# Optimization experiments

Hardware: AMD Instinct MI355X
Metric: run time of the kernel (lower is better)

Reference implementation:

```python
import jax, jax.numpy as jnp
import numpy as np

B, S, D = 2, 2048, 2048
H, KV, HD = 32, 8, 64
REP = H // KV
THETA = 10000.0


def _rope_tables(seq_len, head_dim, dtype):
    inv_freq = 1.0 / (THETA ** (jnp.arange(0, head_dim, 2, dtype=jnp.float32) / head_dim))
    t = jnp.arange(seq_len, dtype=jnp.float32)
    freqs = jnp.outer(t, inv_freq)  # [S, HD/2]
    return jnp.cos(freqs).astype(dtype), jnp.sin(freqs).astype(dtype)


def _apply_rope(x, cos, sin):
    # x: [B, S, nh, HD]; cos/sin: [S, HD/2] -> broadcast [1, S, 1, HD/2]
    c = cos[None, :, None, :]
    s = sin[None, :, None, :]
    x1, x2 = x[..., : HD // 2], x[..., HD // 2:]
    return jnp.concatenate([x1 * c - x2 * s, x1 * s + x2 * c], axis=-1)


def setup_inputs() -> dict:
    key = jax.random.key(0)
    ks = jax.random.split(key, 5)
    x = jax.random.normal(ks[0], (B, S, D), dtype=jnp.float32)
    wq = jax.random.normal(ks[1], (D, H * HD), dtype=jnp.float32) * 0.02
    wk = jax.random.normal(ks[2], (D, KV * HD), dtype=jnp.float32) * 0.02
    wv = jax.random.normal(ks[3], (D, KV * HD), dtype=jnp.float32) * 0.02
    wo = jax.random.normal(ks[4], (H * HD, D), dtype=jnp.float32) * 0.02
    return {"x": x, "wq": wq, "wk": wk, "wv": wv, "wo": wo}


def reference(x, wq, wk, wv, wo):
    b, s, _ = x.shape
    q = (x @ wq).reshape(b, s, H, HD)
    k = (x @ wk).reshape(b, s, KV, HD)
    v = (x @ wv).reshape(b, s, KV, HD)

    cos, sin = _rope_tables(s, HD, x.dtype)
    q = _apply_rope(q, cos, sin)
    k = _apply_rope(k, cos, sin)

    # GQA: group query heads by KV head instead of repeating K/V (same math).
    qg = q.reshape(b, s, KV, REP, HD)  # [B,S,G,R,HD]
    scale = HD ** -0.5
    # scores: [B, G, R, Sq, Sk]
    scores = jnp.einsum("bsgrd,btgd->bgrst", qg, k) * scale
    causal = jnp.tril(jnp.ones((s, s), dtype=bool))
    scores = jnp.where(causal[None, None, None], scores, jnp.finfo(scores.dtype).min)
    probs = jax.nn.softmax(scores, axis=-1)
    out = jnp.einsum("bgrst,btgd->bsgrd", probs, v)  # [B,S,G,R,HD]
    out = out.reshape(b, s, H * HD)
    return out @ wo
```

## Files before the change

kernel.cpp:

```cpp
#include <hip/hip_runtime.h>

#define S_LEN 2048
#define NH 32
#define NKV 8
#define HEADD 64
#define DMODEL 2048
#define NQKV 3072

typedef float f32x4 __attribute__((ext_vector_type(4)));
typedef float f32x16 __attribute__((ext_vector_type(16)));
typedef short s16x8 __attribute__((ext_vector_type(8)));
typedef int   i32x4 __attribute__((ext_vector_type(4)));
typedef unsigned short u16;
typedef u16 u16x4 __attribute__((ext_vector_type(4)));

__device__ __forceinline__ float b2f(u16 u) {
  unsigned int x = ((unsigned int)u) << 16;
  float f;
  __builtin_memcpy(&f, &x, 4);
  return f;
}
__device__ __forceinline__ u16 f2b(float f) {
  unsigned int x;
  __builtin_memcpy(&x, &f, 4);
  unsigned int r = x + 0x7fffu + ((x >> 16) & 1u);
  return (u16)(r >> 16);
}
__device__ __forceinline__ unsigned fbits(float f) {
  unsigned x; __builtin_memcpy(&x, &f, 4); return x;
}

__device__ __forceinline__ void gload_lds16(const u16* g, u16* l) {
  __builtin_amdgcn_global_load_lds((const __attribute__((address_space(1))) void*)g,
                                   (__attribute__((address_space(3))) void*)l, 16, 0, 0);
}

template<int N> __device__ __forceinline__ void wait_vm() {
  asm volatile("s_waitcnt vmcnt(%0)" :: "n"(N) : "memory");
}

__global__ void cast_x_kernel(const float* __restrict__ src, u16* __restrict__ dst) {
  int i = (blockIdx.x * 256 + threadIdx.x) * 4;
  f32x4 v = *(const f32x4*)(src + i);
  u16x4 o;
  o[0] = f2b(v[0]); o[1] = f2b(v[1]); o[2] = f2b(v[2]); o[3] = f2b(v[3]);
  *(u16x4*)(dst + i) = o;
}

__global__ void transpose_cast(const float* __restrict__ src, u16* __restrict__ dst, int N, int K) {
  __shared__ float tile[32][33];
  int n0 = blockIdx.x * 32, k0 = blockIdx.y * 32;
  int tx = threadIdx.x, ty = threadIdx.y;
#pragma unroll
  for (int i = 0; i < 32; i += 8)
    tile[ty + i][tx] = src[(size_t)(k0 + ty + i) * N + n0 + tx];
  __syncthreads();
#pragma unroll
  for (int i = 0; i < 32; i += 8)
    dst[(size_t)(n0 + ty + i) * K + k0 + tx] = f2b(tile[tx][ty + i]);
}

#define PIPE_BODY(Q, STAGE, VMN)                                                   \
  {                                                                                \
    wait_vm<VMN>();                                                                \
    __builtin_amdgcn_s_barrier();                                                  \
    __builtin_amdgcn_sched_barrier(0);                                             \
    if (STAGE) {                                                                   \
      u16* db = sm + ((Q + 3) & 3) * BUFE;                                         \
      gload_lds16(gA0, db + w * 1024);                                             \
      gload_lds16(gA1, db + w * 1024 + 512);                                       \
      if (BN == 256) {                                                             \
        gload_lds16(gB0, db + ABUF + w * 1024);                                    \
        gload_lds16(gB1, db + ABUF + w * 1024 + 512);                              \
      } else {                                                                     \
        gload_lds16(gB0, db + ABUF + w * 512);                                     \
      }                                                                            \
      gA0 += 32; gA1 += 32; gB0 += 32; if (BN == 256) gB1 += 32;                   \
    }                                                                              \
    const u16* bb = sm + Q * BUFE;                                                 \
    s16x8 af[8], bf[NF];                                                           \
    _Pragma("unroll") for (int i = 0; i < 8; i++)  af[i] = *(const s16x8*)(bb + aoff[i]); \
    _Pragma("unroll") for (int j = 0; j < NF; j++) bf[j] = *(const s16x8*)(bb + boff[j]); \
    __builtin_amdgcn_s_setprio(1);                                                 \
    _Pragma("unroll") for (int mi = 0; mi < 8; mi++)                               \
      _Pragma("unroll") for (int ni = 0; ni < NF; ni++)                            \
        acc[mi][ni] = __builtin_amdgcn_mfma_f32_16x16x32_bf16(af[mi], bf[ni], acc[mi][ni], 0, 0, 0); \
    __builtin_amdgcn_s_setprio(0);                                                 \
  }

template<int BN>
__global__ __launch_bounds__(512, 2) void gemm_pipe(
    const u16* __restrict__ A, const u16* __restrict__ Bt, void* __restrict__ Cout,
    int M, int N, int writeF32) {
  extern __shared__ __align__(16) u16 sm[];
  constexpr int NF   = BN / 64;
  constexpr int ABUF = 256 * 32;
  constexpr int BUFE = ABUF + BN * 32;
  constexpr int LPS  = 2 + BN / 128;

  int nb = N / BN;
  int nwg = (M >> 8) * nb;
  int cpx = nwg >> 3;
  int bid = ((int)blockIdx.x & 7) * cpx + ((int)blockIdx.x >> 3);
  int m0 = (bid / nb) << 8;
  int n0 = (bid % nb) * BN;

  int tid = threadIdx.x;
  int lane = tid & 63;
  int w = tid >> 6;
  int wm8 = (w >> 2) << 7;
  int wn8 = (w & 3) * (BN / 4);
  int l15 = lane & 15;
  int quad = lane >> 4;

  int lr = lane >> 3;
  int lc = lane & 7;
  int slot = lc ^ lr;
  int kc8 = (slot & 3) << 3;
  const u16* gA0 = A + (size_t)(m0 + w * 32 + (lr << 1) + (slot >> 2)) * 2048 + kc8;
  const u16* gA1 = gA0 + (size_t)16 * 2048;
  const u16* gB0;
  const u16* gB1;
  if (BN == 256) {
    gB0 = Bt + (size_t)(n0 + w * 32 + (lr << 1) + (slot >> 2)) * 2048 + kc8;
    gB1 = gB0 + (size_t)16 * 2048;
  } else {
    gB0 = Bt + (size_t)(n0 + w * 16 + (lr << 1) + (slot >> 2)) * 2048 + kc8;
    gB1 = gB0;
  }

  int rb = l15 >> 1;
  int sl = (((((l15 & 1) << 2) | quad) ^ rb)) << 3;
  int rbase = rb * 64 + sl;
  int aoff[8], boff[NF];
#pragma unroll
  for (int i = 0; i < 8; i++) aoff[i] = wm8 * 32 + i * 512 + rbase;
#pragma unroll
  for (int j = 0; j < NF; j++) boff[j] = ABUF + wn8 * 32 + j * 512 + rbase;

  f32x4 acc[8][NF] = {};

#pragma unroll
  for (int pt = 0; pt < 3; pt++) {
    u16* db = sm + pt * BUFE;
    gload_lds16(gA0, db + w * 1024);
    gload_lds16(gA1, db + w * 1024 + 512);
    if (BN == 256) {
      gload_lds16(gB0, db + ABUF + w * 1024);
      gload_lds16(gB1, db + ABUF + w * 1024 + 512);
    } else {
      gload_lds16(gB0, db + ABUF + w * 512);
    }
    gA0 += 32; gA1 += 32; gB0 += 32; if (BN == 256) gB1 += 32;
  }

#pragma unroll 1
  for (int it = 0; it < 15; ++it) {
    PIPE_BODY(0, 1, 2 * LPS)
    PIPE_BODY(1, 1, 2 * LPS)
    PIPE_BODY(2, 1, 2 * LPS)
    PIPE_BODY(3, 1, 2 * LPS)
  }
  PIPE_BODY(0, 1, 2 * LPS)
  PIPE_BODY(1, 0, 2 * LPS)
  PIPE_BODY(2, 0, LPS)
  PIPE_BODY(3, 0, 0)

#pragma unroll
  for (int mi = 0; mi < 8; mi++)
#pragma unroll
    for (int ni = 0; ni < NF; ni++)
#pragma unroll
      for (int r = 0; r < 4; r++) {
        int row = m0 + wm8 + mi * 16 + (quad << 2) + r;
        int col = n0 + wn8 + ni * 16 + l15;
        float v = acc[mi][ni][r];
        if (writeF32) ((float*)Cout)[(size_t)row * N + col] = v;
        else ((u16*)Cout)[(size_t)row * N + col] = f2b(v);
      }
}

__global__ void rope_kernel(u16* __restrict__ qkv) {
  int row = blockIdx.x;
  int s = row & (S_LEN - 1);
  u16* p = qkv + (size_t)row * NQKV;
  int t = threadIdx.x;
  int d = t & 31;
  int hh = t >> 5;
  float inv_freq = exp2f(-(float)d * (13.287712379549449f / 32.0f));
  float ang = (float)s * inv_freq;
  float sn, cs;
  sincosf(ang, &sn, &cs);
  const float QSCALE = 0.18033688011112042f;
#pragma unroll
  for (int i = 0; i < 4; i++) {
    int base = (hh + (i << 3)) * HEADD + d;
    float x1 = b2f(p[base]);
    float x2 = b2f(p[base + 32]);
    p[base]      = f2b((x1 * cs - x2 * sn) * QSCALE);
    p[base + 32] = f2b((x1 * sn + x2 * cs) * QSCALE);
  }
  {
    int base = DMODEL + hh * HEADD + d;
    float x1 = b2f(p[base]);
    float x2 = b2f(p[base + 32]);
    p[base]      = f2b(x1 * cs - x2 * sn);
    p[base + 32] = f2b(x1 * sn + x2 * cs);
  }
}

__global__ void vtrans_kernel(const u16* __restrict__ qkv, u16* __restrict__ Vt) {
  __shared__ __align__(16) u16 tile[64][72];
  int bid = blockIdx.x;
  int st = bid & 31;
  int g  = (bid >> 5) & 7;
  int b  = bid >> 8;
  int tid = threadIdx.x;
  int r = tid >> 2;
  int c = (tid & 3) << 4;
  const u16* src = qkv + (size_t)(b * S_LEN + st * 64 + r) * NQKV + 2560 + g * 64 + c;
  *(i32x4*)&tile[r][c]     = *(const i32x4*)src;
  *(i32x4*)&tile[r][c + 8] = *(const i32x4*)(src + 8);
  __syncthreads();
  u16* dst = Vt + (size_t)((b * 8 + g) * 64 + r) * S_LEN + st * 64 + c;
  u16 tmp[16];
#pragma unroll
  for (int j = 0; j < 16; j++) tmp[j] = tile[c + j][r];
  *(i32x4*)dst       = *(i32x4*)&tmp[0];
  *(i32x4*)(dst + 8) = *(i32x4*)&tmp[8];
}

__global__ __launch_bounds__(64) void kvpack_kernel(const u16* __restrict__ qkv,
                                                    const u16* __restrict__ Vt,
                                                    u16* __restrict__ Kp,
                                                    u16* __restrict__ Vp) {
  int bid = blockIdx.x;
  int kb = bid & 63;
  int bg = bid >> 6;
  int g = bg & 7;
  int b = bg >> 3;
  int lane = threadIdx.x;
  int l31 = lane & 31;
  int h2 = lane >> 5;

  const u16* kq = qkv + (size_t)(b * S_LEN + kb * 32 + l31) * NQKV + DMODEL + g * 64 + h2 * 8;
  u16* kdst = Kp + ((size_t)bid * 4) * 512 + lane * 8;
#pragma unroll
  for (int t = 0; t < 4; t++)
    *(i32x4*)(kdst + t * 512) = *(const i32x4*)(kq + t * 16);

  const u16* vq = Vt + (size_t)(bg * 64 + l31) * S_LEN + kb * 32 + h2 * 8;
  u16* vdst = Vp + ((size_t)bid * 4) * 512 + lane * 8;
  *(i32x4*)(vdst)        = *(const i32x4*)vq;
  *(i32x4*)(vdst + 512)  = *(const i32x4*)(vq + 16);
  *(i32x4*)(vdst + 1024) = *(const i32x4*)(vq + (size_t)32 * S_LEN);
  *(i32x4*)(vdst + 1536) = *(const i32x4*)(vq + (size_t)32 * S_LEN + 16);
}

__global__ __launch_bounds__(64) void attn_kernel(const u16* __restrict__ qkv,
                                                  const u16* __restrict__ Kp,
                                                  const u16* __restrict__ Vp,
                                                  u16* __restrict__ out) {
  int bid = blockIdx.x;
  int bh = bid & 63;
  int pr = bid >> 6;
  int h = bh & 31;
  int b = bh >> 5;
  int g = h >> 2;
  int bg = b * 8 + g;
  int lane = threadIdx.x;
  int l31 = lane & 31;
  int h2 = lane >> 5;

  const u16* kp = Kp + ((size_t)bg * 64) * 2048 + lane * 8;
  const u16* vp = Vp + ((size_t)bg * 64) * 2048 + lane * 8;

#pragma unroll 1
  for (int pass = 0; pass < 2; ++pass) {
    int qb = pass ? pr : (63 - pr);
    int q0 = qb << 5;

    const u16* qp = qkv + (size_t)(b * S_LEN + q0 + l31) * NQKV + h * HEADD + h2 * 8;
    s16x8 qf[4];
#pragma unroll
    for (int t = 0; t < 4; t++) qf[t] = *(const s16x8*)(qp + t * 16);

    float l_i = 0.f;
    f32x16 acc[2] = {};

    s16x8 kfa[4], vfa[4], kfb[4], vfb[4];

    auto loadkv = [&](int kb, s16x8 (&kf)[4], s16x8 (&vf)[4]) {
      const u16* kpp = kp + (size_t)kb * 2048;
      const u16* vpp = vp + (size_t)kb * 2048;
#pragma unroll
      for (int t = 0; t < 4; t++) {
        kf[t] = *(const s16x8*)(kpp + t * 512);
        vf[t] = *(const s16x8*)(vpp + t * 512);
      }
    };

    auto compute = [&](int kb, s16x8 (&kf)[4], s16x8 (&vf)[4]) {
      f32x16 sc = {};
      __builtin_amdgcn_s_setprio(1);
#pragma unroll
      for (int t = 0; t < 4; t++)
        sc = __builtin_amdgcn_mfma_f32_32x32x16_bf16(kf[t], qf[t], sc, 0, 0, 0);
      __builtin_amdgcn_s_setprio(0);

      float sv[16];
#pragma unroll
      for (int j = 0; j < 16; j++) sv[j] = sc[j];

      if (kb == qb) {
        int qg = q0 + l31;
#pragma unroll
        for (int j = 0; j < 16; j++) {
          int kg = kb * 32 + (j & 3) + ((j >> 2) << 3) + (h2 << 2);
          if (kg > qg) sv[j] = -1e30f;
        }
      }

      float e[16];
#pragma unroll
      for (int j = 0; j < 16; j++) e[j] = __builtin_amdgcn_exp2f(sv[j]);

      float ps = (((e[0] + e[1]) + (e[2] + e[3])) + ((e[4] + e[5]) + (e[6] + e[7])))
               + (((e[8] + e[9]) + (e[10] + e[11])) + ((e[12] + e[13]) + (e[14] + e[15])));
      ps += __shfl_xor(ps, 32);
      l_i += ps;

      unsigned Pk[8], Ex[8];
#pragma unroll
      for (int r = 0; r < 8; r++) {
        unsigned pk;
        asm("v_cvt_pk_bf16_f32 %0, %1, %2" : "=v"(pk) : "v"(e[2 * r]), "v"(e[2 * r + 1]));
        Pk[r] = pk;
      }
#pragma unroll
      for (int r = 0; r < 8; r++) Ex[r] = (unsigned)__shfl_xor((int)Pk[r], 32);

      unsigned B0u[4], B1u[4];
      B0u[0] = h2 ? Ex[2] : Pk[0];
      B0u[1] = h2 ? Ex[3] : Pk[1];
      B0u[2] = h2 ? Pk[2] : Ex[0];
      B0u[3] = h2 ? Pk[3] : Ex[1];
      B1u[0] = h2 ? Ex[6] : Pk[4];
      B1u[1] = h2 ? Ex[7] : Pk[5];
      B1u[2] = h2 ? Pk[6] : Ex[4];
      B1u[3] = h2 ? Pk[7] : Ex[5];
      s16x8 B0, B1;
      __builtin_memcpy(&B0, B0u, 16);
      __builtin_memcpy(&B1, B1u, 16);

      __builtin_amdgcn_s_setprio(1);
      acc[0] = __builtin_amdgcn_mfma_f32_32x32x16_bf16(vf[0], B0, acc[0], 0, 0, 0);
      acc[0] = __builtin_amdgcn_mfma_f32_32x32x16_bf16(vf[1], B1, acc[0], 0, 0, 0);
      acc[1] = __builtin_amdgcn_mfma_f32_32x32x16_bf16(vf[2], B0, acc[1], 0, 0, 0);
      acc[1] = __builtin_amdgcn_mfma_f32_32x32x16_bf16(vf[3], B1, acc[1], 0, 0, 0);
      __builtin_amdgcn_s_setprio(0);
    };

    loadkv(0, kfa, vfa);
    int kb = 0;
    while (true) {
      if (kb < qb) loadkv(kb + 1, kfb, vfb);
      compute(kb, kfa, vfa);
      if (++kb > qb) break;
      if (kb < qb) loadkv(kb + 1, kfa, vfa);
      compute(kb, kfb, vfb);
      if (++kb > qb) break;
    }

    float linv = 1.0f / l_i;
    u16* op = out + (size_t)(b * S_LEN + q0 + l31) * DMODEL + h * HEADD;
#pragma unroll
    for (int dt = 0; dt < 2; dt++)
#pragma unroll
      for (int rg = 0; rg < 4; rg++) {
        u16x4 t4;
#pragma unroll
        for (int j = 0; j < 4; j++) t4[j] = f2b(acc[dt][rg * 4 + j] * linv);
        *(u16x4*)(op + dt * 32 + rg * 8 + h2 * 4) = t4;
      }
  }
}

extern "C" void kernel_launch(void* const* d_in, const int* in_sizes, int n_in,
                              void* d_out, int out_size, void* d_ws, size_t ws_size,
                              hipStream_t stream) {
  const float* x  = (const float*)d_in[0];
  const float* wq = (const float*)d_in[1];
  const float* wk = (const float*)d_in[2];
  const float* wv = (const float*)d_in[3];
  const float* wo = (const float*)d_in[4];

  char* ws = (char*)d_ws;
  u16* xb    = (u16*)ws;
  u16* wqkvT = (u16*)(ws + 16777216);
  u16* woT   = (u16*)(ws + 16777216 + 12582912);
  u16* qkv   = (u16*)(ws + 16777216 + 12582912 + 8388608);
  u16* attnb = xb;
  u16* Vt    = wqkvT;
  u16* Kp    = (u16*)(ws + 16777216 + 4194304);
  u16* Vp    = (u16*)(ws + 16777216 + 8388608);

  hipFuncSetAttribute(reinterpret_cast<const void*>(gemm_pipe<256>),
                      hipFuncAttributeMaxDynamicSharedMemorySize, 131072);
  hipFuncSetAttribute(reinterpret_cast<const void*>(gemm_pipe<128>),
                      hipFuncAttributeMaxDynamicSharedMemorySize, 98304);

  cast_x_kernel<<<8192, 256, 0, stream>>>(x, xb);
  dim3 tb(32, 8);
  transpose_cast<<<dim3(64, 64), tb, 0, stream>>>(wq, wqkvT, 2048, 2048);
  transpose_cast<<<dim3(16, 64), tb, 0, stream>>>(wk, wqkvT + (size_t)2048 * 2048, 512, 2048);
  transpose_cast<<<dim3(16, 64), tb, 0, stream>>>(wv, wqkvT + (size_t)2560 * 2048, 512, 2048);
  transpose_cast<<<dim3(64, 64), tb, 0, stream>>>(wo, woT, 2048, 2048);

  gemm_pipe<256><<<192, 512, 131072, stream>>>(xb, wqkvT, qkv, 4096, NQKV, 0);
  rope_kernel<<<4096, 256, 0, stream>>>(qkv);
  vtrans_kernel<<<512, 256, 0, stream>>>(qkv, Vt);
  kvpack_kernel<<<1024, 64, 0, stream>>>(qkv, Vt, Kp, Vp);
  attn_kernel<<<2048, 64, 0, stream>>>(qkv, Kp, Vp, attnb);
  gemm_pipe<128><<<256, 512, 98304, stream>>>(attnb, woT, d_out, 4096, 2048, 1);
}
```

Measured before the change: 311.1 us.

## Split attention key range across two waves with LDS reduction

Each attention block now has two wavefronts that take the lower and upper halves of the causal key-block range for the same query tile, roughly halving the serial loop length per wave. After the loop, the second wave writes its partial accumulators and row sums to shared memory and the first wave adds them, normalises and stores the output. The reduction is a plain sum with no rescaling, which appears to rely on the softmax using no running-max correction. The change adds two barriers, about 8 KB of LDS per block and doubled register demand per block, in exchange for more parallelism on the long causal rows.

```diff
diff --git a/kernel.cpp b/kernel.cpp
--- a/kernel.cpp
+++ b/kernel.cpp
@@ -257,10 +257,12 @@
   *(i32x4*)(vdst + 1536) = *(const i32x4*)(vq + (size_t)32 * S_LEN + 16);
 }
 
-__global__ __launch_bounds__(64) void attn_kernel(const u16* __restrict__ qkv,
-                                                  const u16* __restrict__ Kp,
-                                                  const u16* __restrict__ Vp,
-                                                  u16* __restrict__ out) {
+__global__ __launch_bounds__(128, 4) void attn_kernel(const u16* __restrict__ qkv,
+                                                      const u16* __restrict__ Kp,
+                                                      const u16* __restrict__ Vp,
+                                                      u16* __restrict__ out) {
+  __shared__ float red[33 * 64];
+
   int bid = blockIdx.x;
   int bh = bid & 63;
   int pr = bid >> 6;
@@ -268,7 +270,9 @@
   int b = bh >> 5;
   int g = h >> 2;
   int bg = b * 8 + g;
-  int lane = threadIdx.x;
+  int tid = threadIdx.x;
+  int wv = tid >> 6;
+  int lane = tid & 63;
   int l31 = lane & 31;
   int h2 = lane >> 5;
 
@@ -279,6 +283,10 @@
   for (int pass = 0; pass < 2; ++pass) {
     int qb = pass ? pr : (63 - pr);
     int q0 = qb << 5;
+    int nt = qb + 1;
+    int h1 = (nt + 1) >> 1;
+    int k_lo = wv ? h1 : 0;
+    int k_hi = wv ? nt : h1;
 
     const u16* qp = qkv + (size_t)(b * S_LEN + q0 + l31) * NQKV + h * HEADD + h2 * 8;
     s16x8 qf[4];
@@ -361,28 +369,45 @@
       __builtin_amdgcn_s_setprio(0);
     };
 
-    loadkv(0, kfa, vfa);
-    int kb = 0;
-    while (true) {
-      if (kb < qb) loadkv(kb + 1, kfb, vfb);
-      compute(kb, kfa, vfa);
-      if (++kb > qb) break;
-      if (kb < qb) loadkv(kb + 1, kfa, vfa);
-      compute(kb, kfb, vfb);
-      if (++kb > qb) break;
+    if (k_lo < k_hi) {
+      loadkv(k_lo, kfa, vfa);
+      int kb = k_lo;
+      while (true) {
+        if (kb + 1 < k_hi) loadkv(kb + 1, kfb, vfb);
+        compute(kb, kfa, vfa);
+        if (++kb >= k_hi) break;
+        if (kb + 1 < k_hi) loadkv(kb + 1, kfa, vfa);
+        compute(kb, kfb, vfb);
+        if (++kb >= k_hi) break;
+      }
     }
 
-    float linv = 1.0f / l_i;
-    u16* op = out + (size_t)(b * S_LEN + q0 + l31) * DMODEL + h * HEADD;
-#pragma unroll
-    for (int dt = 0; dt < 2; dt++)
-#pragma unroll
-      for (int rg = 0; rg < 4; rg++) {
-        u16x4 t4;
-#pragma unroll
-        for (int j = 0; j < 4; j++) t4[j] = f2b(acc[dt][rg * 4 + j] * linv);
-        *(u16x4*)(op + dt * 32 + rg * 8 + h2 * 4) = t4;
-      }
+    __syncthreads();
+    if (wv) {
+#pragma unroll
+      for (int dt = 0; dt < 2; dt++)
+#pragma unroll
+        for (int j = 0; j < 16; j++) red[(dt * 16 + j) * 64 + lane] = acc[dt][j];
+      red[32 * 64 + lane] = l_i;
+    }
+    __syncthreads();
+    if (!wv) {
+#pragma unroll
+      for (int dt = 0; dt < 2; dt++)
+#pragma unroll
+        for (int j = 0; j < 16; j++) acc[dt][j] += red[(dt * 16 + j) * 64 + lane];
+      float linv = 1.0f / (l_i + red[32 * 64 + lane]);
+      u16* op = out + (size_t)(b * S_LEN + q0 + l31) * DMODEL + h * HEADD;
+#pragma unroll
+      for (int dt = 0; dt < 2; dt++)
+#pragma unroll
+        for (int rg = 0; rg < 4; rg++) {
+          u16x4 t4;
+#pragma unroll
+          for (int j = 0; j < 4; j++) t4[j] = f2b(acc[dt][rg * 4 + j] * linv);
+          *(u16x4*)(op + dt * 32 + rg * 8 + h2 * 4) = t4;
+        }
+    }
   }
 }
 
@@ -421,6 +446,6 @@
   rope_kernel<<<4096, 256, 0, stream>>>(qkv);
   vtrans_kernel<<<512, 256, 0, stream>>>(qkv, Vt);
   kvpack_kernel<<<1024, 64, 0, stream>>>(qkv, Vt, Kp, Vp);
-  attn_kernel<<<2048, 64, 0, stream>>>(qkv, Kp, Vp, attnb);
+  attn_kernel<<<2048, 128, 0, stream>>>(qkv, Kp, Vp, attnb);
   gemm_pipe<128><<<256, 512, 98304, stream>>>(attnb, woT, d_out, 4096, 2048, 1);
 }
```

Measured after the change: 484.8 us. 1.56x slower.
